# Optimization experiments

Measured on AMD Instinct MI355X. Metric: run time of the kernel, lower is better.

Reference implementation:

```python
import jax, jax.numpy as jnp
import numpy as np
from jax.scipy.special import xlogy

NUM_TTA = 64
FILTER_VIEWS = 0.1
KEPT_VIEWS = int(FILTER_VIEWS * NUM_TTA)  # 6
EPS = 1e-8


def setup_inputs() -> dict:
    key = jax.random.key(0)
    k1, k2 = jax.random.split(key)
    x = jax.random.normal(k1, (16384, 4096), dtype=jnp.float32)
    W = jax.random.normal(k2, (4096, 1000), dtype=jnp.float32) * 0.02
    b = jnp.zeros((1000,), dtype=jnp.float32)
    return {"x": x, "W": W, "b": b}


def reference(x, W, b):
    # inner model: linear + softmax -> per-view class probabilities
    probs = jax.nn.softmax(x @ W + b, axis=-1)            # (B*V, C)
    C = probs.shape[-1]
    B = probs.shape[0] // NUM_TTA
    probs = probs.reshape(B, NUM_TTA, C)                  # (b v c)

    # entr(p).sum(-1) == -sum p*log p (entr(0)=0 handled by xlogy)
    entropies = -xlogy(probs, probs).sum(-1)              # (B, V)
    conf_idx = jnp.argsort(entropies, axis=-1)            # most confident first
    votes = jnp.argmax(probs, axis=-1)                    # (B, V)
    sorted_votes = jnp.take_along_axis(votes, conf_idx, axis=1)  # (B, V)

    # initial majority vote over the KEPT_VIEWS most confident views
    counts = jax.nn.one_hot(sorted_votes[:, :KEPT_VIEWS], C, dtype=jnp.float32).sum(1)  # (B, C)

    rows = jnp.arange(B)

    # sequential tie-breaking: while there is a tie at the max, add the next
    # most confident view's vote; at most NUM_TTA - KEPT_VIEWS extra views.
    def body(i, counts):
        maximum = counts.max(axis=-1, keepdims=True)       # (B, 1)
        tied = (counts == maximum).sum(axis=-1) > 1        # (B,)
        cls = sorted_votes[:, KEPT_VIEWS + i]              # (B,)
        return counts.at[rows, cls].add(tied.astype(counts.dtype))

    counts = jax.lax.fori_loop(0, NUM_TTA - KEPT_VIEWS, body, counts)

    predictions = counts / NUM_TTA
    return jnp.log(predictions + EPS)
```

## Files before the change

kernel.cpp:

```cpp
#include <hip/hip_runtime.h>
#include <cstdint>
#include <cstddef>
#include <math.h>

#define M_ROWS 16384
#define N_COLS 1000
#define N_PAD  1024
#define K_DIM  4096
#define NUM_TTA 64
#define KEPT 6
#define BATCH 256
#define CHUNK_MAX 16384
#define NKT (K_DIM / 32)

typedef __attribute__((ext_vector_type(8))) short short8;
typedef __attribute__((ext_vector_type(4))) float v4f;

#define GL_LDS16(g, l)                                                        \
    __builtin_amdgcn_global_load_lds(                                         \
        (const __attribute__((address_space(1))) unsigned int*)(g),           \
        (__attribute__((address_space(3))) unsigned int*)(l), 16, 0, 0)

__device__ __forceinline__ unsigned short bf_rn(float x) {
    unsigned int u = __float_as_uint(x);
    return (unsigned short)((u + 0x7fffu + ((u >> 16) & 1u)) >> 16);
}
__device__ __forceinline__ void split2(float x, unsigned short& h, unsigned short& l) {
    h = bf_rn(x);
    float hf = __uint_as_float(((unsigned int)h) << 16);
    l = bf_rn(x - hf);
}

__global__ __launch_bounds__(1024)
void split_w(const float* __restrict__ W, unsigned short* __restrict__ Wh,
             unsigned short* __restrict__ Wl)
{
    __shared__ float tile[32][33];
    const int k0 = blockIdx.x * 32, n0 = blockIdx.y * 32;
    const int tx = threadIdx.x, ty = threadIdx.y;
    const int n = n0 + tx, k = k0 + ty;
    tile[ty][tx] = (n < N_COLS) ? W[(size_t)k * N_COLS + n] : 0.f;
    __syncthreads();
    const float w = tile[tx][ty];
    unsigned short h, l;
    split2(w, h, l);
    const size_t o = (size_t)(n0 + ty) * K_DIM + k0 + tx;
    Wh[o] = h; Wl[o] = l;
}

__global__ __launch_bounds__(256)
void split_a(const float* __restrict__ x, unsigned short* __restrict__ Ah,
             unsigned short* __restrict__ Al, long long nelem)
{
    const long long i = ((long long)blockIdx.x * 256 + threadIdx.x) * 4;
    if (i >= nelem) return;
    const float4 v = *(const float4*)(x + i);
    unsigned short h0, h1, h2, h3, l0, l1, l2, l3;
    split2(v.x, h0, l0); split2(v.y, h1, l1);
    split2(v.z, h2, l2); split2(v.w, h3, l3);
    ushort4 hv = {h0, h1, h2, h3}, lv = {l0, l1, l2, l3};
    *(ushort4*)(Ah + i) = hv;
    *(ushort4*)(Al + i) = lv;
}

__global__ __launch_bounds__(512, 2)
void gemm_mfma(const unsigned short* __restrict__ Ah, const unsigned short* __restrict__ Al,
               const unsigned short* __restrict__ Bh, const unsigned short* __restrict__ Bl,
               const float* __restrict__ bias, float* __restrict__ logits,
               int m_tiles)
{
    __shared__ __attribute__((aligned(16))) char smem[2 * 4 * 16384];

    const int t    = threadIdx.x;
    const int lane = t & 63;
    const int wave = t >> 6;
    const int wr   = wave >> 2;
    const int wc   = wave & 3;
    const int ml   = lane & 15;
    const int kh   = lane >> 4;

    const int bid  = blockIdx.x;
    const int xcd  = bid & 7;
    const int slot = bid >> 3;
    const int mt   = xcd * (m_tiles >> 3) + (slot >> 2);
    const int nt   = slot & 3;
    const int m0 = mt * 256, n0 = nt * 256;

    const int    schunk = (t & 3) ^ ((t >> 3) & 3);
    const size_t ro     = (size_t)(t >> 2) * (K_DIM * 2) + (size_t)schunk * 16;
    const char* gAh = (const char*)Ah + (size_t)m0 * (K_DIM * 2) + ro;
    const char* gAl = (const char*)Al + (size_t)m0 * (K_DIM * 2) + ro;
    const char* gBh = (const char*)Bh + (size_t)n0 * (K_DIM * 2) + ro;
    const char* gBl = (const char*)Bl + (size_t)n0 * (K_DIM * 2) + ro;
    char* ldst = smem + t * 16;
    const size_t RSTEP = (size_t)128 * K_DIM * 2;

    const int swz = ((kh ^ (ml >> 1)) & 3) << 4;
    const int lbA = wr * 8192 + ml * 64 + swz;
    const int lbB = wc * 4096 + ml * 64 + swz;

    v4f acc[8][4];
#pragma unroll
    for (int i = 0; i < 8; ++i)
#pragma unroll
        for (int j = 0; j < 4; ++j) acc[i][j] = (v4f){0.f, 0.f, 0.f, 0.f};

#define STAGE(WB, KT) do {                                                    \
    const int kb_ = (KT) * 64;                                                \
    char* d_ = ldst + (WB) * 65536;                                           \
    GL_LDS16(gAh + kb_, d_);                GL_LDS16(gAh + RSTEP + kb_, d_ + 8192);  \
    GL_LDS16(gAl + kb_, d_ + 16384);        GL_LDS16(gAl + RSTEP + kb_, d_ + 24576); \
    GL_LDS16(gBh + kb_, d_ + 32768);        GL_LDS16(gBh + RSTEP + kb_, d_ + 40960); \
    GL_LDS16(gBl + kb_, d_ + 49152);        GL_LDS16(gBl + RSTEP + kb_, d_ + 57344); \
} while (0)

#define FRAG(P) (*(const short8*)(smem + (P)))

    STAGE(0, 0);
    asm volatile("s_waitcnt vmcnt(0)" ::: "memory");
    __builtin_amdgcn_s_barrier();

    short8 ah[4], al[4], bh0[2], bl0[2], bh1[2], bl1[2];

#define MFMA3(AI, NI, AH, AL, BH, BL)                                          \
    acc[AI][NI] = __builtin_amdgcn_mfma_f32_16x16x32_bf16(AH, BL, acc[AI][NI], 0, 0, 0); \
    acc[AI][NI] = __builtin_amdgcn_mfma_f32_16x16x32_bf16(AL, BH, acc[AI][NI], 0, 0, 0); \
    acc[AI][NI] = __builtin_amdgcn_mfma_f32_16x16x32_bf16(AH, BH, acc[AI][NI], 0, 0, 0)

#define TILE_STEP(KT, RB) do {                                                \
    const int B0 = (RB) * 65536;                                              \
    \
    if ((KT) + 1 < NKT) STAGE((RB) ^ 1, (KT) + 1);                            \
    _Pragma("unroll")                                                         \
    for (int mf = 0; mf < 4; ++mf) {                                          \
        ah[mf] = FRAG(B0 +         mf * 1024 + lbA);                          \
        al[mf] = FRAG(B0 + 16384 + mf * 1024 + lbA);                          \
    }                                                                         \
    _Pragma("unroll")                                                         \
    for (int nf = 0; nf < 2; ++nf) {                                          \
        bh0[nf] = FRAG(B0 + 32768 + nf * 1024 + lbB);                         \
        bl0[nf] = FRAG(B0 + 49152 + nf * 1024 + lbB);                         \
    }                                                                         \
    __builtin_amdgcn_s_barrier();                                             \
    asm volatile("s_waitcnt lgkmcnt(0)");                                     \
    __builtin_amdgcn_s_setprio(1);                                            \
    _Pragma("unroll")                                                         \
    for (int mf = 0; mf < 4; ++mf) {                                          \
        MFMA3(mf, 0, ah[mf], al[mf], bh0[0], bl0[0]);                         \
        MFMA3(mf, 1, ah[mf], al[mf], bh0[1], bl0[1]);                         \
    }                                                                         \
    __builtin_amdgcn_s_setprio(0);                                            \
    __builtin_amdgcn_s_barrier();                                             \
    \
    _Pragma("unroll")                                                         \
    for (int nf = 0; nf < 2; ++nf) {                                          \
        bh1[nf] = FRAG(B0 + 32768 + (2 + nf) * 1024 + lbB);                   \
        bl1[nf] = FRAG(B0 + 49152 + (2 + nf) * 1024 + lbB);                   \
    }                                                                         \
    __builtin_amdgcn_s_barrier();                                             \
    asm volatile("s_waitcnt lgkmcnt(0)");                                     \
    __builtin_amdgcn_s_setprio(1);                                            \
    _Pragma("unroll")                                                         \
    for (int mf = 0; mf < 4; ++mf) {                                          \
        MFMA3(mf, 2, ah[mf], al[mf], bh1[0], bl1[0]);                         \
        MFMA3(mf, 3, ah[mf], al[mf], bh1[1], bl1[1]);                         \
    }                                                                         \
    __builtin_amdgcn_s_setprio(0);                                            \
    __builtin_amdgcn_s_barrier();                                             \
    \
    _Pragma("unroll")                                                         \
    for (int mf = 0; mf < 4; ++mf) {                                          \
        ah[mf] = FRAG(B0 + 4096 +         mf * 1024 + lbA);                   \
        al[mf] = FRAG(B0 + 16384 + 4096 + mf * 1024 + lbA);                   \
    }                                                                         \
    __builtin_amdgcn_s_barrier();                                             \
    asm volatile("s_waitcnt lgkmcnt(0)");                                     \
    __builtin_amdgcn_s_setprio(1);                                            \
    _Pragma("unroll")                                                         \
    for (int mf = 0; mf < 4; ++mf) {                                          \
        MFMA3(4 + mf, 2, ah[mf], al[mf], bh1[0], bl1[0]);                     \
        MFMA3(4 + mf, 3, ah[mf], al[mf], bh1[1], bl1[1]);                     \
    }                                                                         \
    __builtin_amdgcn_s_setprio(0);                                            \
    __builtin_amdgcn_s_barrier();                                             \
    \
    __builtin_amdgcn_s_setprio(1);                                            \
    _Pragma("unroll")                                                         \
    for (int mf = 0; mf < 4; ++mf) {                                          \
        MFMA3(4 + mf, 0, ah[mf], al[mf], bh0[0], bl0[0]);                     \
        MFMA3(4 + mf, 1, ah[mf], al[mf], bh0[1], bl0[1]);                     \
    }                                                                         \
    __builtin_amdgcn_s_setprio(0);                                            \
    __builtin_amdgcn_sched_barrier(0);                                        \
    asm volatile("s_waitcnt vmcnt(0)" ::: "memory");                          \
    __builtin_amdgcn_s_barrier();                                             \
} while (0)

#pragma unroll 1
    for (int kt = 0; kt < NKT; kt += 2) {
        TILE_STEP(kt, 0);
        TILE_STEP(kt + 1, 1);
    }

#pragma unroll
    for (int mi = 0; mi < 8; ++mi) {
        const int rbase = m0 + wr * 128 + (mi >> 2) * 64 + (mi & 3) * 16 + kh * 4;
#pragma unroll
        for (int ni = 0; ni < 4; ++ni) {
            const int col = n0 + wc * 64 + ni * 16 + ml;
            if (col < N_COLS) {
                const float bv = bias[col];
#pragma unroll
                for (int r = 0; r < 4; ++r)
                    logits[(size_t)(rbase + r) * N_COLS + col] = acc[mi][ni][r] + bv;
            }
        }
    }
#undef TILE_STEP
#undef MFMA3
#undef FRAG
#undef STAGE
}

__global__ __launch_bounds__(256)
void row_stats(const float* __restrict__ logits, double* __restrict__ ent,
               int* __restrict__ votes, int v_base)
{
    __shared__ float  srow[N_COLS];
    __shared__ float  redv[256];
    __shared__ int    redi[256];
    __shared__ double redS[256];
    __shared__ double redT[256];

    const int t = threadIdx.x;
    const float* row = logits + (size_t)blockIdx.x * N_COLS;

    float bv = -3.0e38f;
    int bi = 0;
    for (int c = t; c < N_COLS; c += 256) {
        const float x = row[c];
        srow[c] = x;
        if (x > bv) { bv = x; bi = c; }
    }
    redv[t] = bv; redi[t] = bi;
    __syncthreads();
    for (int s = 128; s > 0; s >>= 1) {
        if (t < s) {
            const float ov = redv[t + s]; const int oi = redi[t + s];
            if (ov > redv[t] || (ov == redv[t] && oi < redi[t])) { redv[t] = ov; redi[t] = oi; }
        }
        __syncthreads();
    }
    const float mx = redv[0];
    const int amax = redi[0];

    double S = 0.0, T = 0.0;
    for (int c = t; c < N_COLS; c += 256) {
        const float d = srow[c] - mx;
        const double e = exp((double)d);
        S += e; T += e * (double)d;
    }
    redS[t] = S; redT[t] = T;
    __syncthreads();
    for (int s = 128; s > 0; s >>= 1) {
        if (t < s) { redS[t] += redS[t + s]; redT[t] += redT[t + s]; }
        __syncthreads();
    }
    if (t == 0) {
        const double Sf = redS[0], Tf = redT[0];
        ent[v_base + blockIdx.x]   = log(Sf) - Tf / Sf;
        votes[v_base + blockIdx.x] = amax;
    }
}

__global__ __launch_bounds__(64)
void vote_kernel(const double* __restrict__ ent, const int* __restrict__ votes,
                 float* __restrict__ out)
{
    __shared__ double e[NUM_TTA];
    __shared__ int    sv[NUM_TTA];
    __shared__ float  counts[N_COLS];

    const int b = blockIdx.x;
    const int t = threadIdx.x;

    e[t] = ent[b * NUM_TTA + t];
    const int myv = votes[b * NUM_TTA + t];
    for (int c = t; c < N_COLS; c += NUM_TTA) counts[c] = 0.f;
    __syncthreads();

    const double et = e[t];
    int rank = 0;
#pragma unroll
    for (int i = 0; i < NUM_TTA; ++i) {
        const double ei = e[i];
        rank += (ei < et) || (ei == et && i < t);
    }
    sv[rank] = myv;
    __syncthreads();

    if (t == 0) {
        for (int j = 0; j < KEPT; ++j) counts[sv[j]] += 1.f;
        float Mv = 0.f; int Tc = 0;
        for (int j = 0; j < KEPT; ++j) {
            const int c = sv[j];
            bool dup = false;
            for (int q = 0; q < j; ++q) dup = dup || (sv[q] == c);
            if (dup) continue;
            const float cv = counts[c];
            if (cv > Mv) { Mv = cv; Tc = 1; }
            else if (cv == Mv) { Tc += 1; }
        }
        for (int i = 0; i < NUM_TTA - KEPT; ++i) {
            if (Tc <= 1) break;
            const int c = sv[KEPT + i];
            const float oldc = counts[c];
            counts[c] = oldc + 1.f;
            if (oldc == Mv)            { Mv += 1.f; Tc = 1; }
            else if (oldc + 1.f == Mv) { Tc += 1; }
        }
    }
    __syncthreads();

    const size_t o0 = (size_t)b * N_COLS;
    for (int c = t; c < N_COLS; c += NUM_TTA)
        out[o0 + c] = logf(counts[c] * (1.f / 64.f) + 1e-8f);
}

extern "C" void kernel_launch(void* const* d_in, const int* in_sizes, int n_in,
                              void* d_out, int out_size, void* d_ws, size_t ws_size,
                              hipStream_t stream) {
    const float* x    = (const float*)d_in[0];
    const float* Wm   = (const float*)d_in[1];
    const float* bias = (const float*)d_in[2];
    float* out = (float*)d_out;

    char* p = (char*)d_ws;
    double* ent  = (double*)p;                     p += (size_t)M_ROWS * 8;
    int*   votes = (int*)p;                        p += (size_t)M_ROWS * 4;
    unsigned short* Wh = (unsigned short*)p;       p += (size_t)N_PAD * K_DIM * 2;
    unsigned short* Wl = (unsigned short*)p;       p += (size_t)N_PAD * K_DIM * 2;
    const size_t base = (size_t)(p - (char*)d_ws);

    long long R = 0;
    if (ws_size > base) R = (long long)((ws_size - base) / (size_t)(8192 + 8192 + 4000));
    R = (R / 2048) * 2048;
    if (R > CHUNK_MAX) R = CHUNK_MAX;
    if (R < 2048) R = 2048;

    unsigned short* Ah = (unsigned short*)p;
    unsigned short* Al = Ah + (size_t)R * K_DIM;
    float* logits = (float*)(Al + (size_t)R * K_DIM);

    split_w<<<dim3(K_DIM / 32, N_PAD / 32), dim3(32, 32), 0, stream>>>(Wm, Wh, Wl);

    for (int m0 = 0; m0 < M_ROWS; m0 += (int)R) {
        const int rows = (int)(((long long)(M_ROWS - m0) < R) ? (M_ROWS - m0) : R);
        const int m_tiles = rows / 256;
        const long long nel = (long long)rows * K_DIM;
        split_a<<<(int)((nel / 4 + 255) / 256), 256, 0, stream>>>(
            x + (size_t)m0 * K_DIM, Ah, Al, nel);
        gemm_mfma<<<4 * m_tiles, 512, 0, stream>>>(
            Ah, Al, Wh, Wl, bias, logits, m_tiles);
        row_stats<<<rows, 256, 0, stream>>>(logits, ent, votes, m0);
    }
    vote_kernel<<<BATCH, NUM_TTA, 0, stream>>>(ent, votes, out);
}
```

Baseline: 768.8 us.

## Cut GEMM barriers per K-tile and make row_stats one wave per row

The GEMM main loop drops most of its intra-tile barriers and lgkmcnt waits. It now issues a single vmcnt wait and barrier at the start of each tile, then loads all B fragments up front so the MFMAs run back-to-back under one priority raise. row_stats is rewritten so each wavefront handles one row with register-held values and shuffle reductions, with no LDS or __syncthreads. It also uses a custom polynomial double exp in place of the library call. The GEMM change removes synchronisation overhead but relies on compiler-inserted LDS waits and a single barrier to keep the double buffer safe.

After: 723.6 us. 1.06x faster.

```diff
diff --git a/kernel.cpp b/kernel.cpp
--- a/kernel.cpp
+++ b/kernel.cpp
@@ -117,8 +117,6 @@
 #define FRAG(P) (*(const short8*)(smem + (P)))
 
     STAGE(0, 0);
-    asm volatile("s_waitcnt vmcnt(0)" ::: "memory");
-    __builtin_amdgcn_s_barrier();
 
     short8 ah[4], al[4], bh0[2], bl0[2], bh1[2], bl1[2];
 
@@ -127,9 +125,11 @@
     acc[AI][NI] = __builtin_amdgcn_mfma_f32_16x16x32_bf16(AL, BH, acc[AI][NI], 0, 0, 0); \
     acc[AI][NI] = __builtin_amdgcn_mfma_f32_16x16x32_bf16(AH, BH, acc[AI][NI], 0, 0, 0)
 
-#define TILE_STEP(KT, RB) do {                                                \
+#define TILE_BODY(KT, RB) do {                                                \
     const int B0 = (RB) * 65536;                                              \
-    \
+    asm volatile("s_waitcnt vmcnt(0)" ::: "memory");                          \
+    __builtin_amdgcn_s_barrier();                                             \
+    __builtin_amdgcn_sched_barrier(0);                                        \
     if ((KT) + 1 < NKT) STAGE((RB) ^ 1, (KT) + 1);                            \
     _Pragma("unroll")                                                         \
     for (int mf = 0; mf < 4; ++mf) {                                          \
@@ -140,66 +140,42 @@
     for (int nf = 0; nf < 2; ++nf) {                                          \
         bh0[nf] = FRAG(B0 + 32768 + nf * 1024 + lbB);                         \
         bl0[nf] = FRAG(B0 + 49152 + nf * 1024 + lbB);                         \
-    }                                                                         \
-    __builtin_amdgcn_s_barrier();                                             \
-    asm volatile("s_waitcnt lgkmcnt(0)");                                     \
+        bh1[nf] = FRAG(B0 + 32768 + (2 + nf) * 1024 + lbB);                   \
+        bl1[nf] = FRAG(B0 + 49152 + (2 + nf) * 1024 + lbB);                   \
+    }                                                                         \
     __builtin_amdgcn_s_setprio(1);                                            \
     _Pragma("unroll")                                                         \
     for (int mf = 0; mf < 4; ++mf) {                                          \
         MFMA3(mf, 0, ah[mf], al[mf], bh0[0], bl0[0]);                         \
         MFMA3(mf, 1, ah[mf], al[mf], bh0[1], bl0[1]);                         \
     }                                                                         \
-    __builtin_amdgcn_s_setprio(0);                                            \
-    __builtin_amdgcn_s_barrier();                                             \
-    \
-    _Pragma("unroll")                                                         \
-    for (int nf = 0; nf < 2; ++nf) {                                          \
-        bh1[nf] = FRAG(B0 + 32768 + (2 + nf) * 1024 + lbB);                   \
-        bl1[nf] = FRAG(B0 + 49152 + (2 + nf) * 1024 + lbB);                   \
-    }                                                                         \
-    __builtin_amdgcn_s_barrier();                                             \
-    asm volatile("s_waitcnt lgkmcnt(0)");                                     \
-    __builtin_amdgcn_s_setprio(1);                                            \
     _Pragma("unroll")                                                         \
     for (int mf = 0; mf < 4; ++mf) {                                          \
         MFMA3(mf, 2, ah[mf], al[mf], bh1[0], bl1[0]);                         \
         MFMA3(mf, 3, ah[mf], al[mf], bh1[1], bl1[1]);                         \
     }                                                                         \
-    __builtin_amdgcn_s_setprio(0);                                            \
-    __builtin_amdgcn_s_barrier();                                             \
-    \
     _Pragma("unroll")                                                         \
     for (int mf = 0; mf < 4; ++mf) {                                          \
         ah[mf] = FRAG(B0 + 4096 +         mf * 1024 + lbA);                   \
         al[mf] = FRAG(B0 + 16384 + 4096 + mf * 1024 + lbA);                   \
     }                                                                         \
-    __builtin_amdgcn_s_barrier();                                             \
-    asm volatile("s_waitcnt lgkmcnt(0)");                                     \
-    __builtin_amdgcn_s_setprio(1);                                            \
     _Pragma("unroll")                                                         \
     for (int mf = 0; mf < 4; ++mf) {                                          \
         MFMA3(4 + mf, 2, ah[mf], al[mf], bh1[0], bl1[0]);                     \
         MFMA3(4 + mf, 3, ah[mf], al[mf], bh1[1], bl1[1]);                     \
     }                                                                         \
-    __builtin_amdgcn_s_setprio(0);                                            \
-    __builtin_amdgcn_s_barrier();                                             \
-    \
-    __builtin_amdgcn_s_setprio(1);                                            \
     _Pragma("unroll")                                                         \
     for (int mf = 0; mf < 4; ++mf) {                                          \
         MFMA3(4 + mf, 0, ah[mf], al[mf], bh0[0], bl0[0]);                     \
         MFMA3(4 + mf, 1, ah[mf], al[mf], bh0[1], bl0[1]);                     \
     }                                                                         \
     __builtin_amdgcn_s_setprio(0);                                            \
-    __builtin_amdgcn_sched_barrier(0);                                        \
-    asm volatile("s_waitcnt vmcnt(0)" ::: "memory");                          \
-    __builtin_amdgcn_s_barrier();                                             \
 } while (0)
 
 #pragma unroll 1
     for (int kt = 0; kt < NKT; kt += 2) {
-        TILE_STEP(kt, 0);
-        TILE_STEP(kt + 1, 1);
+        TILE_BODY(kt, 0);
+        TILE_BODY(kt + 1, 1);
     }
 
 #pragma unroll
@@ -216,60 +192,79 @@
             }
         }
     }
-#undef TILE_STEP
+#undef TILE_BODY
 #undef MFMA3
 #undef FRAG
 #undef STAGE
 }
 
+__device__ __forceinline__ double exp_neg(double d) {
+    if (d < -700.0) return 0.0;
+    const double kd = rint(d * 1.4426950408889634074);
+    double r = fma(-kd, 6.93147180369123816490e-01, d);
+    r = fma(-kd, 1.90821492927058770002e-10, r);
+    double p = 2.08767569878680989792e-09;
+    p = fma(p, r, 2.50521083854417187751e-08);
+    p = fma(p, r, 2.75573192239858906526e-07);
+    p = fma(p, r, 2.75573192239858925110e-06);
+    p = fma(p, r, 2.48015873015873015873e-05);
+    p = fma(p, r, 1.98412698412698412526e-04);
+    p = fma(p, r, 1.38888888888888894069e-03);
+    p = fma(p, r, 8.33333333333333321769e-03);
+    p = fma(p, r, 4.16666666666666643537e-02);
+    p = fma(p, r, 1.66666666666666657415e-01);
+    p = fma(p, r, 5.0e-01);
+    p = fma(p, r, 1.0);
+    p = fma(p, r, 1.0);
+    const long long k = (long long)kd;
+    return p * __longlong_as_double((1023LL + k) << 52);
+}
+
 __global__ __launch_bounds__(256)
 void row_stats(const float* __restrict__ logits, double* __restrict__ ent,
                int* __restrict__ votes, int v_base)
 {
-    __shared__ float  srow[N_COLS];
-    __shared__ float  redv[256];
-    __shared__ int    redi[256];
-    __shared__ double redS[256];
-    __shared__ double redT[256];
-
-    const int t = threadIdx.x;
-    const float* row = logits + (size_t)blockIdx.x * N_COLS;
-
-    float bv = -3.0e38f;
-    int bi = 0;
-    for (int c = t; c < N_COLS; c += 256) {
-        const float x = row[c];
-        srow[c] = x;
+    const int lane = threadIdx.x & 63;
+    const int wave = threadIdx.x >> 6;
+    const int row  = blockIdx.x * 4 + wave;
+    const float* rp = logits + (size_t)row * N_COLS;
+
+    float v[16];
+    float bv = -3.0e38f; int bi = 0;
+#pragma unroll
+    for (int j = 0; j < 16; ++j) {
+        const int c = j * 64 + lane;
+        const float x = (c < N_COLS) ? rp[c] : -3.0e38f;
+        v[j] = x;
         if (x > bv) { bv = x; bi = c; }
     }
-    redv[t] = bv; redi[t] = bi;
-    __syncthreads();
-    for (int s = 128; s > 0; s >>= 1) {
-        if (t < s) {
-            const float ov = redv[t + s]; const int oi = redi[t + s];
-            if (ov > redv[t] || (ov == redv[t] && oi < redi[t])) { redv[t] = ov; redi[t] = oi; }
+#pragma unroll
+    for (int s = 32; s > 0; s >>= 1) {
+        const float ov = __shfl_xor(bv, s);
+        const int   oi = __shfl_xor(bi, s);
+        if (ov > bv || (ov == bv && oi < bi)) { bv = ov; bi = oi; }
+    }
+    const float mx = bv;
+    const int amax = bi;
+
+    double S = 0.0, T = 0.0;
+#pragma unroll
+    for (int j = 0; j < 16; ++j) {
+        const int c = j * 64 + lane;
+        if (c < N_COLS) {
+            const float d = v[j] - mx;
+            const double e = exp_neg((double)d);
+            S += e; T += e * (double)d;
         }
-        __syncthreads();
-    }
-    const float mx = redv[0];
-    const int amax = redi[0];
-
-    double S = 0.0, T = 0.0;
-    for (int c = t; c < N_COLS; c += 256) {
-        const float d = srow[c] - mx;
-        const double e = exp((double)d);
-        S += e; T += e * (double)d;
-    }
-    redS[t] = S; redT[t] = T;
-    __syncthreads();
-    for (int s = 128; s > 0; s >>= 1) {
-        if (t < s) { redS[t] += redS[t + s]; redT[t] += redT[t + s]; }
-        __syncthreads();
-    }
-    if (t == 0) {
-        const double Sf = redS[0], Tf = redT[0];
-        ent[v_base + blockIdx.x]   = log(Sf) - Tf / Sf;
-        votes[v_base + blockIdx.x] = amax;
+    }
+#pragma unroll
+    for (int s = 32; s > 0; s >>= 1) {
+        S += __shfl_xor(S, s);
+        T += __shfl_xor(T, s);
+    }
+    if (lane == 0) {
+        ent[v_base + row]   = log(S) - T / S;
+        votes[v_base + row] = amax;
     }
 }
 
@@ -362,7 +357,7 @@
             x + (size_t)m0 * K_DIM, Ah, Al, nel);
         gemm_mfma<<<4 * m_tiles, 512, 0, stream>>>(
             Ah, Al, Wh, Wl, bias, logits, m_tiles);
-        row_stats<<<rows, 256, 0, stream>>>(logits, ent, votes, m0);
+        row_stats<<<rows / 4, 256, 0, stream>>>(logits, ent, votes, m0);
     }
     vote_kernel<<<BATCH, NUM_TTA, 0, stream>>>(ent, votes, out);
 }
```
